# Performance work log

Measured on AMD Instinct MI355X. Metric: run time of the kernel, lower is better.

Reference implementation:

```python
import jax, jax.numpy as jnp
import numpy as np

WINDOW = 16
NUM_HEADS = 4
DIM = 256
LN_EPS = 1e-5


def setup_inputs() -> dict:
    key = jax.random.key(0)
    ks = jax.random.split(key, 8)
    B, C, N = 8, DIM, 16384
    s = 1.0 / np.sqrt(C)
    x = jax.random.normal(ks[0], (B, C, N), dtype=jnp.float32)
    in_proj_w = jax.random.uniform(ks[1], (3 * C, C), minval=-s, maxval=s, dtype=jnp.float32)
    in_proj_b = jnp.zeros((3 * C,), dtype=jnp.float32)
    out_proj_w = jax.random.uniform(ks[2], (C, C), minval=-s, maxval=s, dtype=jnp.float32)
    out_proj_b = jnp.zeros((C,), dtype=jnp.float32)
    ln_g = jnp.ones((C,), dtype=jnp.float32)
    ln_b = jnp.zeros((C,), dtype=jnp.float32)
    return {"x": x, "in_proj_w": in_proj_w, "in_proj_b": in_proj_b,
            "out_proj_w": out_proj_w, "out_proj_b": out_proj_b,
            "ln_g": ln_g, "ln_b": ln_b}


def _swin_attn_1d(x, in_proj_w, in_proj_b, out_proj_w, out_proj_b, ln_g, ln_b):
    B, C, N = x.shape
    W = WINDOW
    H = NUM_HEADS
    hd = C // H
    xt = jnp.transpose(x, (0, 2, 1))                      # [B, N, C]
    pad_len = (W - N % W) % W                             # static Python int
    if pad_len > 0:
        xt = jnp.pad(xt, ((0, 0), (0, pad_len), (0, 0)))
    N_pad = N + pad_len
    nw = B * (N_pad // W)
    xw = xt.reshape(nw, W, C)                             # [nw, W, C]
    # QKV projection (torch MHA: x @ in_proj_w.T + in_proj_b)
    qkv = jnp.einsum('nwc,dc->nwd', xw, in_proj_w) + in_proj_b  # [nw, W, 3C]
    q, k, v = jnp.split(qkv, 3, axis=-1)
    q = q.reshape(nw, W, H, hd) * (1.0 / np.sqrt(hd))
    k = k.reshape(nw, W, H, hd)
    v = v.reshape(nw, W, H, hd)
    scores = jnp.einsum('nqhd,nkhd->nhqk', q, k)          # [nw, H, W, W]
    probs = jax.nn.softmax(scores, axis=-1)
    attn = jnp.einsum('nhqk,nkhd->nqhd', probs, v).reshape(nw, W, C)
    attn = jnp.einsum('nwc,dc->nwd', attn, out_proj_w) + out_proj_b
    # residual + LayerNorm
    y = attn + xw
    mu = jnp.mean(y, axis=-1, keepdims=True)
    var = jnp.mean(jnp.square(y - mu), axis=-1, keepdims=True)
    y = (y - mu) * jax.lax.rsqrt(var + LN_EPS) * ln_g + ln_b
    y = y.reshape(B, N_pad, C)
    if pad_len > 0:
        y = y[:, :N, :]
    return jnp.transpose(y, (0, 2, 1))                    # [B, C, N]


def reference(x, in_proj_w, in_proj_b, out_proj_w, out_proj_b, ln_g, ln_b):
    return _swin_attn_1d(x, in_proj_w, in_proj_b, out_proj_w, out_proj_b, ln_g, ln_b)
```

## Files before the change

### kernel.cpp

```cpp
#include <hip/hip_runtime.h>


#define C_DIM 256
#define NSEQ  16384

typedef __attribute__((ext_vector_type(8))) short bf16x8;
typedef __attribute__((ext_vector_type(4))) float f32x4;

__device__ __forceinline__ unsigned short f2bf(float f) {
    unsigned int u = __builtin_bit_cast(unsigned int, f);
    u += 0x7FFFu + ((u >> 16) & 1u);
    return (unsigned short)(u >> 16);
}
__device__ __forceinline__ float bf2f(unsigned short h) {
    unsigned int u = ((unsigned int)h) << 16;
    return __builtin_bit_cast(float, u);
}
__device__ __forceinline__ unsigned int pack2(float a, float b) {
    return ((unsigned int)f2bf(b) << 16) | (unsigned int)f2bf(a);
}

__global__ void prep_weights(const float* __restrict__ wq_f, const float* __restrict__ wo_f,
                             unsigned short* __restrict__ wq, unsigned short* __restrict__ wo) {
    int i = blockIdx.x * 256 + threadIdx.x;
    if (i < 768 * 256) wq[i] = f2bf(wq_f[i]);
    if (i < 256 * 256) wo[i] = f2bf(wo_f[i]);
}

__global__ __launch_bounds__(512, 4) void swin_fused(
    const float* __restrict__ x,
    const unsigned short* __restrict__ wq,
    const unsigned short* __restrict__ wo,
    const float* __restrict__ bq,
    const float* __restrict__ bo,
    const float* __restrict__ lng,
    const float* __restrict__ lnb,
    float* __restrict__ out)
{
    __shared__ __align__(16) unsigned short lds_x[32][264];
    __shared__ __align__(16) unsigned short lds_qk[32][520];
    __shared__ __align__(16) unsigned short lds_vt[256][40];
    __shared__ __align__(16) unsigned short lds_p[8][16][16];
    __shared__ float lds_mean[32];
    __shared__ float lds_rstd[32];

    const int tid  = threadIdx.x;
    const int wv   = tid >> 6;
    const int lane = tid & 63;
    const int l15  = lane & 15;
    const int quad = lane >> 4;

    const int w0    = blockIdx.x * 2;
    const int batch = w0 >> 10;
    const int nbase = (w0 & 1023) << 4;
    const long xbase = (long)batch * ((long)C_DIM * NSEQ) + nbase;

    {
        const int t4 = (tid & 7) << 2;
        const int c4 = (tid >> 3) << 2;
        float4 r[4];
        #pragma unroll
        for (int j = 0; j < 4; ++j)
            r[j] = *reinterpret_cast<const float4*>(&x[xbase + (long)(c4 + j) * NSEQ + t4]);
        const float* rf = reinterpret_cast<const float*>(r);
        #pragma unroll
        for (int i = 0; i < 4; ++i) {
            uint2 v;
            v.x = pack2(rf[0 * 4 + i], rf[1 * 4 + i]);
            v.y = pack2(rf[2 * 4 + i], rf[3 * 4 + i]);
            *reinterpret_cast<uint2*>(&lds_x[t4 + i][c4]) = v;
        }
    }
    __syncthreads();

    for (int i = 0; i < 6; ++i) {
        const int nt = (i << 3) + wv;
        const int d  = nt * 16 + l15;
        const unsigned short* wrow = wq + d * 256 + quad * 8;
        bf16x8 bfr[8];
        #pragma unroll
        for (int k = 0; k < 8; ++k)
            bfr[k] = *reinterpret_cast<const bf16x8*>(wrow + k * 32);
        const float bias = bq[d];
        f32x4 acc0 = {bias, bias, bias, bias};
        f32x4 acc1 = {bias, bias, bias, bias};
        #pragma unroll
        for (int k = 0; k < 8; ++k) {
            bf16x8 a0 = *reinterpret_cast<const bf16x8*>(&lds_x[l15][k * 32 + quad * 8]);
            bf16x8 a1 = *reinterpret_cast<const bf16x8*>(&lds_x[16 + l15][k * 32 + quad * 8]);
            acc0 = __builtin_amdgcn_mfma_f32_16x16x32_bf16(a0, bfr[k], acc0, 0, 0, 0);
            acc1 = __builtin_amdgcn_mfma_f32_16x16x32_bf16(a1, bfr[k], acc1, 0, 0, 0);
        }
        if (d < 512) {
            #pragma unroll
            for (int r = 0; r < 4; ++r) {
                lds_qk[quad * 4 + r][d]      = f2bf(acc0[r]);
                lds_qk[16 + quad * 4 + r][d] = f2bf(acc1[r]);
            }
        } else {
            #pragma unroll
            for (int r = 0; r < 4; ++r) {
                lds_vt[d - 512][quad * 4 + r]      = f2bf(acc0[r]);
                lds_vt[d - 512][16 + quad * 4 + r] = f2bf(acc1[r]);
            }
        }
    }
    __syncthreads();

    {
        const int g = wv >> 2;
        const int h = wv & 3;
        f32x4 sc = {0.f, 0.f, 0.f, 0.f};
        #pragma unroll
        for (int kk = 0; kk < 2; ++kk) {
            bf16x8 aq = *reinterpret_cast<const bf16x8*>(&lds_qk[g*16 + l15][h*64 + kk*32 + quad*8]);
            bf16x8 bk = *reinterpret_cast<const bf16x8*>(&lds_qk[g*16 + l15][256 + h*64 + kk*32 + quad*8]);
            sc = __builtin_amdgcn_mfma_f32_16x16x32_bf16(aq, bk, sc, 0, 0, 0);
        }
        #pragma unroll
        for (int r = 0; r < 4; ++r) {
            float s = sc[r] * 0.125f;
            float m = s;
            #pragma unroll
            for (int msk = 1; msk <= 8; msk <<= 1) m = fmaxf(m, __shfl_xor(m, msk, 16));
            float e = __expf(s - m);
            float su = e;
            #pragma unroll
            for (int msk = 1; msk <= 8; msk <<= 1) su += __shfl_xor(su, msk, 16);
            lds_p[wv][quad * 4 + r][l15] = f2bf(e / su);
        }
        bf16x8 ap = {0,0,0,0,0,0,0,0};
        if (quad < 2) ap = *reinterpret_cast<const bf16x8*>(&lds_p[wv][l15][quad * 8]);
        #pragma unroll
        for (int dt = 0; dt < 4; ++dt) {
            bf16x8 bv = {0,0,0,0,0,0,0,0};
            if (quad < 2)
                bv = *reinterpret_cast<const bf16x8*>(&lds_vt[h*64 + dt*16 + l15][g*16 + quad*8]);
            f32x4 acc = {0.f, 0.f, 0.f, 0.f};
            acc = __builtin_amdgcn_mfma_f32_16x16x32_bf16(ap, bv, acc, 0, 0, 0);
            #pragma unroll
            for (int r = 0; r < 4; ++r)
                lds_qk[g*16 + quad*4 + r][h*64 + dt*16 + l15] = f2bf(acc[r]);
        }
    }
    __syncthreads();

    unsigned short* ldy = &lds_vt[0][0];
    for (int i = 0; i < 2; ++i) {
        const int nt = (i << 3) + wv;
        const int d  = nt * 16 + l15;
        const unsigned short* wrow = wo + d * 256 + quad * 8;
        bf16x8 bfr[8];
        #pragma unroll
        for (int k = 0; k < 8; ++k)
            bfr[k] = *reinterpret_cast<const bf16x8*>(wrow + k * 32);
        const float bias = bo[d];
        f32x4 acc0 = {bias, bias, bias, bias};
        f32x4 acc1 = {bias, bias, bias, bias};
        #pragma unroll
        for (int k = 0; k < 8; ++k) {
            bf16x8 a0 = *reinterpret_cast<const bf16x8*>(&lds_qk[l15][k * 32 + quad * 8]);
            bf16x8 a1 = *reinterpret_cast<const bf16x8*>(&lds_qk[16 + l15][k * 32 + quad * 8]);
            acc0 = __builtin_amdgcn_mfma_f32_16x16x32_bf16(a0, bfr[k], acc0, 0, 0, 0);
            acc1 = __builtin_amdgcn_mfma_f32_16x16x32_bf16(a1, bfr[k], acc1, 0, 0, 0);
        }
        #pragma unroll
        for (int r = 0; r < 4; ++r) {
            const int r0 = quad * 4 + r;
            ldy[r0 * 264 + d]        = f2bf(acc0[r] + bf2f(lds_x[r0][d]));
            ldy[(16 + r0) * 264 + d] = f2bf(acc1[r] + bf2f(lds_x[16 + r0][d]));
        }
    }
    __syncthreads();

    {
        const int row = tid >> 4, part = tid & 15;
        float s = 0.f, sq = 0.f;
        #pragma unroll
        for (int half = 0; half < 2; ++half) {
            bf16x8 yv = *reinterpret_cast<const bf16x8*>(&ldy[row * 264 + part * 16 + half * 8]);
            #pragma unroll
            for (int ii = 0; ii < 8; ++ii) {
                float v = bf2f((unsigned short)yv[ii]);
                s += v; sq += v * v;
            }
        }
        #pragma unroll
        for (int msk = 1; msk <= 8; msk <<= 1) {
            s  += __shfl_xor(s,  msk, 16);
            sq += __shfl_xor(sq, msk, 16);
        }
        if (part == 0) {
            float mean = s * (1.0f / 256.0f);
            float var  = sq * (1.0f / 256.0f) - mean * mean;
            lds_mean[row] = mean;
            lds_rstd[row] = rsqrtf(var + 1e-5f);
        }
    }
    __syncthreads();

    {
        const int t4 = (tid & 7) << 2;
        const int c0 = tid >> 3;
        float mean[4], rstd[4];
        #pragma unroll
        for (int i = 0; i < 4; ++i) { mean[i] = lds_mean[t4 + i]; rstd[i] = lds_rstd[t4 + i]; }
        #pragma unroll
        for (int it = 0; it < 4; ++it) {
            const int c = c0 + (it << 6);
            const float g = lng[c], b = lnb[c];
            float4 o;
            float* of = reinterpret_cast<float*>(&o);
            #pragma unroll
            for (int i = 0; i < 4; ++i)
                of[i] = (bf2f(ldy[(t4 + i) * 264 + c]) - mean[i]) * rstd[i] * g + b;
            *reinterpret_cast<float4*>(&out[xbase + (long)c * NSEQ + t4]) = o;
        }
    }
}

extern "C" void kernel_launch(void* const* d_in, const int* in_sizes, int n_in,
                              void* d_out, int out_size, void* d_ws, size_t ws_size,
                              hipStream_t stream) {
    const float* x   = (const float*)d_in[0];
    const float* ipw = (const float*)d_in[1];
    const float* ipb = (const float*)d_in[2];
    const float* opw = (const float*)d_in[3];
    const float* opb = (const float*)d_in[4];
    const float* lng = (const float*)d_in[5];
    const float* lnb = (const float*)d_in[6];
    float* out = (float*)d_out;

    unsigned short* wq = (unsigned short*)d_ws;
    unsigned short* wo = wq + 768 * 256;

    prep_weights<<<768, 256, 0, stream>>>(ipw, opw, wq, wo);
    swin_fused<<<4096, 512, 0, stream>>>(x, wq, wo, ipb, opb, lng, lnb, out);
}
```

Measured before the change: 433.9 us.

## Pre-tile weights for coalesced fragment loads, swizzle LDS, hoist A fragments

The weight prep kernel now writes the bf16 weights in MFMA-fragment-tiled order, so each wave's B-fragment loads read contiguous memory instead of strided rows. LDS rows are XOR-swizzled to reduce bank conflicts. The activation A-fragments are loaded into registers once and reused across the output tiles, and the first weight fragment load is issued before the barrier so it overlaps the x staging. Keeping those fragments in registers raises register pressure under the 512x4 launch bounds and could cause spills.

```diff
diff --git a/kernel.cpp b/kernel.cpp
--- a/kernel.cpp
+++ b/kernel.cpp
@@ -19,12 +19,25 @@
 __device__ __forceinline__ unsigned int pack2(float a, float b) {
     return ((unsigned int)f2bf(b) << 16) | (unsigned int)f2bf(a);
 }
+__device__ __forceinline__ int xsw(int row, int col) {
+    return col ^ (((row >> 3) & 1) << 4);
+}
 
 __global__ void prep_weights(const float* __restrict__ wq_f, const float* __restrict__ wo_f,
                              unsigned short* __restrict__ wq, unsigned short* __restrict__ wo) {
     int i = blockIdx.x * 256 + threadIdx.x;
-    if (i < 768 * 256) wq[i] = f2bf(wq_f[i]);
-    if (i < 256 * 256) wo[i] = f2bf(wo_f[i]);
+    if (i < 768 * 256) {
+        int nt = i >> 12, r = i & 4095;
+        int k = r >> 9, r2 = r & 511;
+        int l = r2 >> 5, r3 = r2 & 31;
+        wq[i] = f2bf(wq_f[(nt * 16 + l) * 256 + k * 32 + r3]);
+    }
+    if (i < 256 * 256) {
+        int nt = i >> 12, r = i & 4095;
+        int k = r >> 9, r2 = r & 511;
+        int l = r2 >> 5, r3 = r2 & 31;
+        wo[i] = f2bf(wo_f[(nt * 16 + l) * 256 + k * 32 + r3]);
+    }
 }
 
 __global__ __launch_bounds__(512, 4) void swin_fused(
@@ -68,34 +81,47 @@
             uint2 v;
             v.x = pack2(rf[0 * 4 + i], rf[1 * 4 + i]);
             v.y = pack2(rf[2 * 4 + i], rf[3 * 4 + i]);
-            *reinterpret_cast<uint2*>(&lds_x[t4 + i][c4]) = v;
-        }
-    }
-    __syncthreads();
+            *reinterpret_cast<uint2*>(&lds_x[t4 + i][xsw(t4 + i, c4)]) = v;
+        }
+    }
+
+    const unsigned short* wqbase = wq + l15 * 32 + quad * 8;
+    bf16x8 bfr[8];
+    #pragma unroll
+    for (int k = 0; k < 8; ++k)
+        bfr[k] = *reinterpret_cast<const bf16x8*>(wqbase + wv * 4096 + k * 512);
+
+    __syncthreads();
+
+    bf16x8 xa0[8], xa1[8];
+    #pragma unroll
+    for (int k = 0; k < 8; ++k) {
+        xa0[k] = *reinterpret_cast<const bf16x8*>(&lds_x[l15][xsw(l15, k * 32 + quad * 8)]);
+        xa1[k] = *reinterpret_cast<const bf16x8*>(&lds_x[16 + l15][xsw(16 + l15, k * 32 + quad * 8)]);
+    }
 
     for (int i = 0; i < 6; ++i) {
         const int nt = (i << 3) + wv;
         const int d  = nt * 16 + l15;
-        const unsigned short* wrow = wq + d * 256 + quad * 8;
-        bf16x8 bfr[8];
-        #pragma unroll
-        for (int k = 0; k < 8; ++k)
-            bfr[k] = *reinterpret_cast<const bf16x8*>(wrow + k * 32);
+        if (i) {
+            #pragma unroll
+            for (int k = 0; k < 8; ++k)
+                bfr[k] = *reinterpret_cast<const bf16x8*>(wqbase + nt * 4096 + k * 512);
+        }
         const float bias = bq[d];
         f32x4 acc0 = {bias, bias, bias, bias};
         f32x4 acc1 = {bias, bias, bias, bias};
         #pragma unroll
         for (int k = 0; k < 8; ++k) {
-            bf16x8 a0 = *reinterpret_cast<const bf16x8*>(&lds_x[l15][k * 32 + quad * 8]);
-            bf16x8 a1 = *reinterpret_cast<const bf16x8*>(&lds_x[16 + l15][k * 32 + quad * 8]);
-            acc0 = __builtin_amdgcn_mfma_f32_16x16x32_bf16(a0, bfr[k], acc0, 0, 0, 0);
-            acc1 = __builtin_amdgcn_mfma_f32_16x16x32_bf16(a1, bfr[k], acc1, 0, 0, 0);
+            acc0 = __builtin_amdgcn_mfma_f32_16x16x32_bf16(xa0[k], bfr[k], acc0, 0, 0, 0);
+            acc1 = __builtin_amdgcn_mfma_f32_16x16x32_bf16(xa1[k], bfr[k], acc1, 0, 0, 0);
         }
         if (d < 512) {
             #pragma unroll
             for (int r = 0; r < 4; ++r) {
-                lds_qk[quad * 4 + r][d]      = f2bf(acc0[r]);
-                lds_qk[16 + quad * 4 + r][d] = f2bf(acc1[r]);
+                const int r0 = quad * 4 + r;
+                lds_qk[r0][xsw(r0, d)]           = f2bf(acc0[r]);
+                lds_qk[16 + r0][xsw(16 + r0, d)] = f2bf(acc1[r]);
             }
         } else {
             #pragma unroll
@@ -113,8 +139,9 @@
         f32x4 sc = {0.f, 0.f, 0.f, 0.f};
         #pragma unroll
         for (int kk = 0; kk < 2; ++kk) {
-            bf16x8 aq = *reinterpret_cast<const bf16x8*>(&lds_qk[g*16 + l15][h*64 + kk*32 + quad*8]);
-            bf16x8 bk = *reinterpret_cast<const bf16x8*>(&lds_qk[g*16 + l15][256 + h*64 + kk*32 + quad*8]);
+            const int row = g * 16 + l15;
+            bf16x8 aq = *reinterpret_cast<const bf16x8*>(&lds_qk[row][xsw(row, h * 64 + kk * 32 + quad * 8)]);
+            bf16x8 bk = *reinterpret_cast<const bf16x8*>(&lds_qk[row][xsw(row, 256 + h * 64 + kk * 32 + quad * 8)]);
             sc = __builtin_amdgcn_mfma_f32_16x16x32_bf16(aq, bk, sc, 0, 0, 0);
         }
         #pragma unroll
@@ -135,40 +162,55 @@
         for (int dt = 0; dt < 4; ++dt) {
             bf16x8 bv = {0,0,0,0,0,0,0,0};
             if (quad < 2)
-                bv = *reinterpret_cast<const bf16x8*>(&lds_vt[h*64 + dt*16 + l15][g*16 + quad*8]);
+                bv = *reinterpret_cast<const bf16x8*>(&lds_vt[h * 64 + dt * 16 + l15][g * 16 + quad * 8]);
             f32x4 acc = {0.f, 0.f, 0.f, 0.f};
             acc = __builtin_amdgcn_mfma_f32_16x16x32_bf16(ap, bv, acc, 0, 0, 0);
             #pragma unroll
-            for (int r = 0; r < 4; ++r)
-                lds_qk[g*16 + quad*4 + r][h*64 + dt*16 + l15] = f2bf(acc[r]);
-        }
-    }
+            for (int r = 0; r < 4; ++r) {
+                const int row = g * 16 + quad * 4 + r;
+                lds_qk[row][xsw(row, h * 64 + dt * 16 + l15)] = f2bf(acc[r]);
+            }
+        }
+    }
+
+    const unsigned short* wobase = wo + l15 * 32 + quad * 8;
+    bf16x8 wfr[8];
+    #pragma unroll
+    for (int k = 0; k < 8; ++k)
+        wfr[k] = *reinterpret_cast<const bf16x8*>(wobase + wv * 4096 + k * 512);
+
     __syncthreads();
 
     unsigned short* ldy = &lds_vt[0][0];
+    bf16x8 aa0[8], aa1[8];
+    #pragma unroll
+    for (int k = 0; k < 8; ++k) {
+        aa0[k] = *reinterpret_cast<const bf16x8*>(&lds_qk[l15][xsw(l15, k * 32 + quad * 8)]);
+        aa1[k] = *reinterpret_cast<const bf16x8*>(&lds_qk[16 + l15][xsw(16 + l15, k * 32 + quad * 8)]);
+    }
     for (int i = 0; i < 2; ++i) {
         const int nt = (i << 3) + wv;
         const int d  = nt * 16 + l15;
-        const unsigned short* wrow = wo + d * 256 + quad * 8;
-        bf16x8 bfr[8];
-        #pragma unroll
-        for (int k = 0; k < 8; ++k)
-            bfr[k] = *reinterpret_cast<const bf16x8*>(wrow + k * 32);
+        if (i) {
+            #pragma unroll
+            for (int k = 0; k < 8; ++k)
+                wfr[k] = *reinterpret_cast<const bf16x8*>(wobase + nt * 4096 + k * 512);
+        }
         const float bias = bo[d];
         f32x4 acc0 = {bias, bias, bias, bias};
         f32x4 acc1 = {bias, bias, bias, bias};
         #pragma unroll
         for (int k = 0; k < 8; ++k) {
-            bf16x8 a0 = *reinterpret_cast<const bf16x8*>(&lds_qk[l15][k * 32 + quad * 8]);
-            bf16x8 a1 = *reinterpret_cast<const bf16x8*>(&lds_qk[16 + l15][k * 32 + quad * 8]);
-            acc0 = __builtin_amdgcn_mfma_f32_16x16x32_bf16(a0, bfr[k], acc0, 0, 0, 0);
-            acc1 = __builtin_amdgcn_mfma_f32_16x16x32_bf16(a1, bfr[k], acc1, 0, 0, 0);
+            acc0 = __builtin_amdgcn_mfma_f32_16x16x32_bf16(aa0[k], wfr[k], acc0, 0, 0, 0);
+            acc1 = __builtin_amdgcn_mfma_f32_16x16x32_bf16(aa1[k], wfr[k], acc1, 0, 0, 0);
         }
         #pragma unroll
         for (int r = 0; r < 4; ++r) {
             const int r0 = quad * 4 + r;
-            ldy[r0 * 264 + d]        = f2bf(acc0[r] + bf2f(lds_x[r0][d]));
-            ldy[(16 + r0) * 264 + d] = f2bf(acc1[r] + bf2f(lds_x[16 + r0][d]));
+            ldy[r0 * 264 + xsw(r0, d)] =
+                f2bf(acc0[r] + bf2f(lds_x[r0][xsw(r0, d)]));
+            ldy[(16 + r0) * 264 + xsw(16 + r0, d)] =
+                f2bf(acc1[r] + bf2f(lds_x[16 + r0][xsw(16 + r0, d)]));
         }
     }
     __syncthreads();
@@ -178,7 +220,7 @@
         float s = 0.f, sq = 0.f;
         #pragma unroll
         for (int half = 0; half < 2; ++half) {
-            bf16x8 yv = *reinterpret_cast<const bf16x8*>(&ldy[row * 264 + part * 16 + half * 8]);
+            bf16x8 yv = *reinterpret_cast<const bf16x8*>(&ldy[row * 264 + xsw(row, part * 16 + half * 8)]);
             #pragma unroll
             for (int ii = 0; ii < 8; ++ii) {
                 float v = bf2f((unsigned short)yv[ii]);
@@ -213,7 +255,7 @@
             float* of = reinterpret_cast<float*>(&o);
             #pragma unroll
             for (int i = 0; i < 4; ++i)
-                of[i] = (bf2f(ldy[(t4 + i) * 264 + c]) - mean[i]) * rstd[i] * g + b;
+                of[i] = (bf2f(ldy[(t4 + i) * 264 + xsw(t4 + i, c)]) - mean[i]) * rstd[i] * g + b;
             *reinterpret_cast<float4*>(&out[xbase + (long)c * NSEQ + t4]) = o;
         }
     }
```

Measured after the change: 368.2 us. 1.18x faster.
